# Kernel tuning notes

Hardware: AMD Instinct MI355X
Metric: run time of the kernel (lower is better)

The kernel has to match this reference:

```python
import jax, jax.numpy as jnp
import numpy as np

IN_CHANNELS = 8
CHANNELS = 8
MASK_OUT_STRIDE = 4


def aligned_bilinear(x, factor):
    # Faithful port of AdelaiDet aligned_bilinear (align_corners=True).
    if factor == 1:
        return x
    n, c, h, w = x.shape
    x = jnp.pad(x, ((0, 0), (0, 0), (0, 1), (0, 1)), mode='edge')
    oh, ow = factor * h + 1, factor * w + 1

    def interp_axis(arr, out_len, axis):
        # align_corners=True from size s+1 -> factor*s+1: src coord = i / factor
        coords = jnp.arange(out_len) / factor
        i0 = jnp.floor(coords).astype(jnp.int32)
        i1 = jnp.minimum(i0 + 1, arr.shape[axis] - 1)
        t = (coords - i0).astype(arr.dtype)
        a0 = jnp.take(arr, i0, axis=axis)
        a1 = jnp.take(arr, i1, axis=axis)
        shp = [1] * arr.ndim
        shp[axis] = out_len
        t = t.reshape(shp)
        return a0 * (1 - t) + a1 * t

    x = interp_axis(x, oh, 2)
    x = interp_axis(x, ow, 3)
    p = factor // 2
    x = jnp.pad(x, ((0, 0), (0, 0), (p, 0), (p, 0)), mode='edge')
    return x[:, :, : oh - 1, : ow - 1]


def setup_inputs() -> dict:
    key = jax.random.key(0)
    ks = jax.random.split(key, 6)
    N, C, H, W = 4, IN_CHANNELS, 112, 200
    n_inst = 200
    stride = 8
    num_gen_params = (C + 2) * CHANNELS + CHANNELS + CHANNELS * CHANNELS + CHANNELS + CHANNELS + 1  # 169
    mask_feats = jax.random.normal(ks[0], (N, C, H, W), dtype=jnp.float32)
    mask_head_params = jax.random.normal(ks[1], (n_inst, num_gen_params), dtype=jnp.float32) * 0.1
    # instance centers anywhere inside the image (in input-image pixel coords)
    instance_locations = jax.random.uniform(ks[2], (n_inst, 2), dtype=jnp.float32) * jnp.array(
        [W * stride, H * stride], dtype=jnp.float32)
    sizes_of_interest = jnp.array([64.0, 128.0, 256.0, 512.0, 1024.0], dtype=jnp.float32)
    im_inds = jax.random.randint(ks[3], (n_inst,), 0, N, dtype=jnp.int32)
    fpn_levels = jax.random.randint(ks[4], (n_inst,), 0, 5, dtype=jnp.int32)
    return {
        'mask_feats': mask_feats,
        'mask_head_params': mask_head_params,
        'instance_locations': instance_locations,
        'sizes_of_interest': sizes_of_interest,
        'im_inds': im_inds,
        'fpn_levels': fpn_levels,
        'mask_feat_stride': stride,
    }


def reference(mask_feats, mask_head_params, instance_locations, sizes_of_interest,
              im_inds, fpn_levels, mask_feat_stride):
    N, C, H, W = mask_feats.shape
    n_inst = mask_head_params.shape[0]
    HW = H * W
    stride = mask_feat_stride  # python int

    # compute_locations: (x, y) pairs, x fastest, at pixel centers (stride//2 offset)
    xs = (jnp.arange(W) * stride + stride // 2).astype(mask_feats.dtype)
    ys = (jnp.arange(H) * stride + stride // 2).astype(mask_feats.dtype)
    gx, gy = jnp.meshgrid(xs, ys, indexing='xy')  # [H, W]
    locations = jnp.stack([gx, gy], axis=-1).reshape(HW, 2)  # [HW, 2]

    # relative coords, normalized by size-of-interest per instance
    rel = instance_locations[:, None, :] - locations[None, :, :]  # [n, HW, 2]
    rel = jnp.transpose(rel, (0, 2, 1))  # [n, 2, HW]
    soi = sizes_of_interest[fpn_levels]  # [n]
    rel = rel / soi[:, None, None]

    feats = mask_feats[im_inds].reshape(n_inst, C, HW)  # [n, C, HW]
    x = jnp.concatenate([rel, feats], axis=1)  # [n, C+2, HW]

    # parse_dynamic_params: split [n, 169] into per-layer 1x1 conv weights/biases
    wn = [(C + 2) * CHANNELS, CHANNELS * CHANNELS, CHANNELS * 1]
    bn = [CHANNELS, CHANNELS, 1]
    sizes = wn + bn
    offs = np.cumsum([0] + sizes)
    parts = [mask_head_params[:, offs[i]:offs[i + 1]] for i in range(len(sizes))]
    w0 = parts[0].reshape(n_inst, CHANNELS, C + 2)
    w1 = parts[1].reshape(n_inst, CHANNELS, CHANNELS)
    w2 = parts[2].reshape(n_inst, 1, CHANNELS)
    b0, b1, b2 = parts[3], parts[4], parts[5]

    # per-instance grouped 1x1 convs == batched matmuls over instances
    x = jax.nn.relu(jnp.einsum('noi,nip->nop', w0, x) + b0[:, :, None])
    x = jax.nn.relu(jnp.einsum('noi,nip->nop', w1, x) + b1[:, :, None])
    x = jnp.einsum('noi,nip->nop', w2, x) + b2[:, :, None]  # [n, 1, HW]

    mask_logits = x.reshape(n_inst, 1, H, W)
    factor = stride // MASK_OUT_STRIDE
    return aligned_bilinear(mask_logits, factor)
```

## Files before the change

kernel.cpp:

```cpp
#include <hip/hip_runtime.h>


#define IN_C   8
#define CHN    8
#define Hh     112
#define Ww     200
#define HWp    (Hh * Ww)
#define OH     224
#define OW     400
#define TY     16
#define RL     9
#define NTILES (OH / TY)
#define NPARAMS 169


__global__ __launch_bounds__(256)
void dmh_fused_kernel(const float* __restrict__ feats,
                      const float* __restrict__ params,
                      const float* __restrict__ iloc,
                      const float* __restrict__ soi_tab,
                      const int*   __restrict__ im_inds,
                      const int*   __restrict__ fpn_levels,
                      float* __restrict__ out)
{
    __shared__ float lds[RL][Ww];

    const int bid  = blockIdx.x;
    const int inst = bid / NTILES;
    const int ty   = bid - inst * NTILES;
    const int y0   = ty * TY;
    const int r_lo = (y0 > 0 ? (y0 - 1) : 0) >> 1;
    const int tid  = threadIdx.x;

    const float* __restrict__ wp = params + inst * NPARAMS;
    const float soi    = soi_tab[fpn_levels[inst]];
    const float inv_s  = 1.0f / soi;
    const float ix     = iloc[inst * 2 + 0];
    const float iy     = iloc[inst * 2 + 1];
    const float* __restrict__ fb = feats + (size_t)im_inds[inst] * (IN_C * HWp);

    const int NG = (RL * Ww) / 4;
    for (int g = tid; g < NG; g += 256) {
        const int rr = g / (Ww / 4);
        const int c4 = (g - rr * (Ww / 4)) * 4;
        const int r  = r_lo + rr;
        const float* fp = fb + r * Ww + c4;

        float fv[IN_C][4];
        #pragma unroll
        for (int ch = 0; ch < IN_C; ch++) {
            const float4 t = *reinterpret_cast<const float4*>(fp + ch * HWp);
            fv[ch][0] = t.x; fv[ch][1] = t.y; fv[ch][2] = t.z; fv[ch][3] = t.w;
        }
        const float in1 = (iy - (float)(r * 8 + 4)) * inv_s;
        float in0[4];
        #pragma unroll
        for (int k = 0; k < 4; k++)
            in0[k] = (ix - (float)((c4 + k) * 8 + 4)) * inv_s;

        float h0[CHN][4];
        #pragma unroll
        for (int o = 0; o < CHN; o++) {
            const float b = wp[152 + o];
            #pragma unroll
            for (int k = 0; k < 4; k++) {
                float a = fmaf(wp[o * 10 + 0], in0[k], b);
                a = fmaf(wp[o * 10 + 1], in1, a);
                #pragma unroll
                for (int i = 0; i < IN_C; i++)
                    a = fmaf(wp[o * 10 + 2 + i], fv[i][k], a);
                h0[o][k] = fmaxf(a, 0.0f);
            }
        }
        float h1[CHN][4];
        #pragma unroll
        for (int o = 0; o < CHN; o++) {
            const float b = wp[160 + o];
            #pragma unroll
            for (int k = 0; k < 4; k++) {
                float a = b;
                #pragma unroll
                for (int i = 0; i < CHN; i++)
                    a = fmaf(wp[80 + o * 8 + i], h0[i][k], a);
                h1[o][k] = fmaxf(a, 0.0f);
            }
        }
        float res[4];
        #pragma unroll
        for (int k = 0; k < 4; k++) {
            float a = wp[168];
            #pragma unroll
            for (int i = 0; i < CHN; i++)
                a = fmaf(wp[144 + i], h1[i][k], a);
            res[k] = a;
        }
        *reinterpret_cast<float4*>(&lds[rr][c4]) =
            make_float4(res[0], res[1], res[2], res[3]);
    }
    __syncthreads();

    float* __restrict__ ob = out + (size_t)inst * (OH * OW);
    const int NQ = (TY * OW) / 4;
    for (int q = tid; q < NQ; q += 256) {
        const int dy = q / (OW / 4);
        const int gx = q - dy * (OW / 4);
        const int x  = gx * 4;
        const int y  = y0 + dy;
        const int i  = (y > 0 ? y - 1 : 0);
        const int rr0 = (i >> 1) - r_lo;
        const int r1g = (i >> 1) + (i & 1);
        const int rr1 = (r1g > Hh - 1 ? Hh - 1 : r1g) - r_lo;
        const float wy1 = (i & 1) ? 0.5f : 0.0f;
        const float wy0 = 1.0f - wy1;

        const int cx  = x >> 1;
        const int cm1 = (cx > 0 ? cx - 1 : 0);
        const float a_m = lds[rr0][cm1], a_0 = lds[rr0][cx], a_p = lds[rr0][cx + 1];
        const float b_m = lds[rr1][cm1], b_0 = lds[rr1][cx], b_p = lds[rr1][cx + 1];
        const float Rm = wy0 * a_m + wy1 * b_m;
        const float R0 = wy0 * a_0 + wy1 * b_0;
        const float Rp = wy0 * a_p + wy1 * b_p;

        float4 o4;
        o4.x = 0.5f * (Rm + R0);
        o4.y = R0;
        o4.z = 0.5f * (R0 + Rp);
        o4.w = Rp;
        *reinterpret_cast<float4*>(&ob[y * OW + x]) = o4;
    }
}

extern "C" void kernel_launch(void* const* d_in, const int* in_sizes, int n_in,
                              void* d_out, int out_size, void* d_ws, size_t ws_size,
                              hipStream_t stream) {
    const float* mask_feats = (const float*)d_in[0];
    const float* params     = (const float*)d_in[1];
    const float* iloc       = (const float*)d_in[2];
    const float* soi        = (const float*)d_in[3];
    const int*   im_inds    = (const int*)d_in[4];
    const int*   fpn        = (const int*)d_in[5];
    float* out = (float*)d_out;

    const int n_inst = in_sizes[4];
    dim3 grid(n_inst * NTILES);
    dim3 block(256);
    hipLaunchKernelGGL(dmh_fused_kernel, grid, block, 0, stream,
                       mask_feats, params, iloc, soi, im_inds, fpn, out);
}
```

Before: 47.55 us.

## Split MLP into two phases with fp16 hidden layer staged in LDS

```diff
diff --git a/kernel.cpp b/kernel.cpp
--- a/kernel.cpp
+++ b/kernel.cpp
@@ -10,11 +10,17 @@
 #define OW     400
 #define TY     16
 #define RL     9
+#define NPIX   (RL * Ww)
+#define NPAIR  (NPIX / 2)
+#define NQUAD  (NPIX / 4)
 #define NTILES (OH / TY)
 #define NPARAMS 169
-
-
-__global__ __launch_bounds__(256)
+#define BLK    256
+
+typedef __fp16 f16x2 __attribute__((ext_vector_type(2)));
+
+
+__global__ __launch_bounds__(BLK, 4)
 void dmh_fused_kernel(const float* __restrict__ feats,
                       const float* __restrict__ params,
                       const float* __restrict__ iloc,
@@ -23,7 +29,8 @@
                       const int*   __restrict__ fpn_levels,
                       float* __restrict__ out)
 {
-    __shared__ float lds[RL][Ww];
+    __shared__ uint  h0s[CHN][NPAIR];
+    __shared__ float lgt[RL][Ww];
 
     const int bid  = blockIdx.x;
     const int inst = bid / NTILES;
@@ -39,69 +46,117 @@
     const float iy     = iloc[inst * 2 + 1];
     const float* __restrict__ fb = feats + (size_t)im_inds[inst] * (IN_C * HWp);
 
-    const int NG = (RL * Ww) / 4;
-    for (int g = tid; g < NG; g += 256) {
-        const int rr = g / (Ww / 4);
-        const int c4 = (g - rr * (Ww / 4)) * 4;
-        const int r  = r_lo + rr;
-        const float* fp = fb + r * Ww + c4;
-
-        float fv[IN_C][4];
-        #pragma unroll
-        for (int ch = 0; ch < IN_C; ch++) {
-            const float4 t = *reinterpret_cast<const float4*>(fp + ch * HWp);
-            fv[ch][0] = t.x; fv[ch][1] = t.y; fv[ch][2] = t.z; fv[ch][3] = t.w;
+    {
+        float w0r[80], b0r[CHN];
+        #pragma unroll
+        for (int i = 0; i < 80; i++) w0r[i] = wp[i];
+        #pragma unroll
+        for (int i = 0; i < CHN; i++) b0r[i] = wp[152 + i];
+        #pragma unroll
+        for (int i = 0; i < 80; i++) asm volatile("" : "+s"(w0r[i]));
+        #pragma unroll
+        for (int i = 0; i < CHN; i++) asm volatile("" : "+s"(b0r[i]));
+
+        for (int g = tid; g < NQUAD; g += BLK) {
+            const int rr = g / (Ww / 4);
+            const int c4 = (g - rr * (Ww / 4)) * 4;
+            const int r  = r_lo + rr;
+            const float* fp = fb + r * Ww + c4;
+
+            float fv[IN_C][4];
+            #pragma unroll
+            for (int ch = 0; ch < IN_C; ch++) {
+                const float4 t = *reinterpret_cast<const float4*>(fp + ch * HWp);
+                fv[ch][0] = t.x; fv[ch][1] = t.y; fv[ch][2] = t.z; fv[ch][3] = t.w;
+            }
+            const float in1 = (iy - (float)(r * 8 + 4)) * inv_s;
+            float in0[4];
+            #pragma unroll
+            for (int k = 0; k < 4; k++)
+                in0[k] = (ix - (float)((c4 + k) * 8 + 4)) * inv_s;
+
+            #pragma unroll
+            for (int o = 0; o < CHN; o++) {
+                const float bo = fmaf(w0r[o * 10 + 1], in1, b0r[o]);
+                float t0 = fmaf(w0r[o * 10 + 0], in0[0], bo);
+                float t1 = fmaf(w0r[o * 10 + 0], in0[1], bo);
+                float t2 = fmaf(w0r[o * 10 + 0], in0[2], bo);
+                float t3 = fmaf(w0r[o * 10 + 0], in0[3], bo);
+                #pragma unroll
+                for (int i = 0; i < IN_C; i++) {
+                    const float w = w0r[o * 10 + 2 + i];
+                    t0 = fmaf(w, fv[i][0], t0);
+                    t1 = fmaf(w, fv[i][1], t1);
+                    t2 = fmaf(w, fv[i][2], t2);
+                    t3 = fmaf(w, fv[i][3], t3);
+                }
+                const f16x2 pa = __builtin_amdgcn_cvt_pkrtz(fmaxf(t0, 0.0f), fmaxf(t1, 0.0f));
+                const f16x2 pb = __builtin_amdgcn_cvt_pkrtz(fmaxf(t2, 0.0f), fmaxf(t3, 0.0f));
+                uint2 u;
+                u.x = *reinterpret_cast<const uint*>(&pa);
+                u.y = *reinterpret_cast<const uint*>(&pb);
+                *reinterpret_cast<uint2*>(&h0s[o][2 * g]) = u;
+            }
         }
-        const float in1 = (iy - (float)(r * 8 + 4)) * inv_s;
-        float in0[4];
-        #pragma unroll
-        for (int k = 0; k < 4; k++)
-            in0[k] = (ix - (float)((c4 + k) * 8 + 4)) * inv_s;
-
-        float h0[CHN][4];
-        #pragma unroll
-        for (int o = 0; o < CHN; o++) {
-            const float b = wp[152 + o];
-            #pragma unroll
-            for (int k = 0; k < 4; k++) {
-                float a = fmaf(wp[o * 10 + 0], in0[k], b);
-                a = fmaf(wp[o * 10 + 1], in1, a);
-                #pragma unroll
-                for (int i = 0; i < IN_C; i++)
-                    a = fmaf(wp[o * 10 + 2 + i], fv[i][k], a);
-                h0[o][k] = fmaxf(a, 0.0f);
-            }
-        }
-        float h1[CHN][4];
-        #pragma unroll
-        for (int o = 0; o < CHN; o++) {
-            const float b = wp[160 + o];
-            #pragma unroll
-            for (int k = 0; k < 4; k++) {
-                float a = b;
-                #pragma unroll
-                for (int i = 0; i < CHN; i++)
-                    a = fmaf(wp[80 + o * 8 + i], h0[i][k], a);
-                h1[o][k] = fmaxf(a, 0.0f);
-            }
-        }
-        float res[4];
-        #pragma unroll
-        for (int k = 0; k < 4; k++) {
-            float a = wp[168];
-            #pragma unroll
-            for (int i = 0; i < CHN; i++)
-                a = fmaf(wp[144 + i], h1[i][k], a);
-            res[k] = a;
-        }
-        *reinterpret_cast<float4*>(&lds[rr][c4]) =
-            make_float4(res[0], res[1], res[2], res[3]);
     }
     __syncthreads();
 
+    {
+        float w1r[64], w2r[CHN], b1r[CHN], b2;
+        #pragma unroll
+        for (int i = 0; i < 64; i++) w1r[i] = wp[80 + i];
+        #pragma unroll
+        for (int i = 0; i < CHN; i++) w2r[i] = wp[144 + i];
+        #pragma unroll
+        for (int i = 0; i < CHN; i++) b1r[i] = wp[160 + i];
+        b2 = wp[168];
+        #pragma unroll
+        for (int i = 0; i < 64; i++) asm volatile("" : "+s"(w1r[i]));
+        #pragma unroll
+        for (int i = 0; i < CHN; i++) asm volatile("" : "+s"(w2r[i]));
+        #pragma unroll
+        for (int i = 0; i < CHN; i++) asm volatile("" : "+s"(b1r[i]));
+        asm volatile("" : "+s"(b2));
+
+        for (int g = tid; g < NQUAD; g += BLK) {
+            float h[IN_C][4];
+            #pragma unroll
+            for (int i = 0; i < CHN; i++) {
+                const uint2 u = *reinterpret_cast<const uint2*>(&h0s[i][2 * g]);
+                const f16x2 pa = *reinterpret_cast<const f16x2*>(&u.x);
+                const f16x2 pb = *reinterpret_cast<const f16x2*>(&u.y);
+                h[i][0] = (float)pa.x; h[i][1] = (float)pa.y;
+                h[i][2] = (float)pb.x; h[i][3] = (float)pb.y;
+            }
+            float r0 = b2, r1 = b2, r2 = b2, r3 = b2;
+            #pragma unroll
+            for (int o = 0; o < CHN; o++) {
+                float a0 = b1r[o], a1 = b1r[o], a2 = b1r[o], a3 = b1r[o];
+                #pragma unroll
+                for (int i = 0; i < CHN; i++) {
+                    const float w = w1r[o * 8 + i];
+                    a0 = fmaf(w, h[i][0], a0);
+                    a1 = fmaf(w, h[i][1], a1);
+                    a2 = fmaf(w, h[i][2], a2);
+                    a3 = fmaf(w, h[i][3], a3);
+                }
+                const float w2 = w2r[o];
+                r0 = fmaf(w2, fmaxf(a0, 0.0f), r0);
+                r1 = fmaf(w2, fmaxf(a1, 0.0f), r1);
+                r2 = fmaf(w2, fmaxf(a2, 0.0f), r2);
+                r3 = fmaf(w2, fmaxf(a3, 0.0f), r3);
+            }
+            const int rr = g / (Ww / 4);
+            const int c4 = (g - rr * (Ww / 4)) * 4;
+            *reinterpret_cast<float4*>(&lgt[rr][c4]) =
+                make_float4(r0, r1, r2, r3);
+        }
+    }
+    __syncthreads();
+
     float* __restrict__ ob = out + (size_t)inst * (OH * OW);
     const int NQ = (TY * OW) / 4;
-    for (int q = tid; q < NQ; q += 256) {
+    for (int q = tid; q < NQ; q += BLK) {
         const int dy = q / (OW / 4);
         const int gx = q - dy * (OW / 4);
         const int x  = gx * 4;
@@ -115,8 +170,8 @@
 
         const int cx  = x >> 1;
         const int cm1 = (cx > 0 ? cx - 1 : 0);
-        const float a_m = lds[rr0][cm1], a_0 = lds[rr0][cx], a_p = lds[rr0][cx + 1];
-        const float b_m = lds[rr1][cm1], b_0 = lds[rr1][cx], b_p = lds[rr1][cx + 1];
+        const float a_m = lgt[rr0][cm1], a_0 = lgt[rr0][cx], a_p = lgt[rr0][cx + 1];
+        const float b_m = lgt[rr1][cm1], b_0 = lgt[rr1][cx], b_p = lgt[rr1][cx + 1];
         const float Rm = wy0 * a_m + wy1 * b_m;
         const float R0 = wy0 * a_0 + wy1 * b_0;
         const float Rp = wy0 * a_p + wy1 * b_p;
@@ -143,7 +198,7 @@
 
     const int n_inst = in_sizes[4];
     dim3 grid(n_inst * NTILES);
-    dim3 block(256);
+    dim3 block(BLK);
     hipLaunchKernelGGL(dmh_fused_kernel, grid, block, 0, stream,
                        mask_feats, params, iloc, soi, im_inds, fpn, out);
 }
```

Result: faster. 39.35 us (-17.3%).
